# Optimization experiments

Hardware: AMD Instinct MI355X
Metric: run time of the kernel (lower is better)

Reference implementation:

```python
import jax, jax.numpy as jnp
import numpy as np

DIM = 1024
HEADS = 16
DIM_HEAD = 64
NUM_FREQS = 16
INNER = HEADS * DIM_HEAD


def rotate_half(x):
    # matches torch: cat((-x[..., 1::2], x[..., ::2]), dim=-1)
    x1 = x[..., ::2]
    x2 = x[..., 1::2]
    return jnp.concatenate((-x2, x1), axis=-1)


def rope_fourier_cache(seq_len, head_dim, num_freqs):
    freqs = 10000.0 ** (-jnp.arange(0, head_dim, 2, dtype=jnp.float32) / head_dim)  # [hd/2]
    pos = jnp.arange(seq_len, dtype=jnp.float32)[:, None]  # [n,1]
    angles = pos * freqs  # [n, hd/2]
    sin = jnp.sin(angles)
    cos = jnp.cos(angles)
    # interleave-duplicate each value per pair: [n, hd]
    sin = jnp.stack([sin, sin], axis=-1).reshape(seq_len, head_dim)
    cos = jnp.stack([cos, cos], axis=-1).reshape(seq_len, head_dim)
    ffreqs = jnp.arange(1, num_freqs + 1, dtype=jnp.float32)  # [F]
    p = jnp.arange(seq_len, dtype=jnp.float32)[:, None]  # [n,1]
    fourier = jnp.concatenate([jnp.sin(p * ffreqs), jnp.cos(p * ffreqs)], axis=-1)  # [n, 2F]
    return sin, cos, fourier


def setup_inputs() -> dict:
    key = jax.random.key(0)
    ks = jax.random.split(key, 6)
    b, n = 4, 2048
    x = jax.random.normal(ks[0], (b, n, DIM), dtype=jnp.float32)
    w_qkv = jax.random.normal(ks[1], (3 * INNER, DIM), dtype=jnp.float32) * (DIM ** -0.5)
    w_fproj = jax.random.normal(ks[2], (DIM_HEAD, 2 * NUM_FREQS), dtype=jnp.float32) * ((2 * NUM_FREQS) ** -0.5)
    b_fproj = jax.random.normal(ks[3], (DIM_HEAD,), dtype=jnp.float32) * 0.02
    w_out = jax.random.normal(ks[4], (DIM, INNER), dtype=jnp.float32) * (INNER ** -0.5)
    b_out = jax.random.normal(ks[5], (DIM,), dtype=jnp.float32) * 0.02
    return {"x": x, "w_qkv": w_qkv, "w_fproj": w_fproj, "b_fproj": b_fproj,
            "w_out": w_out, "b_out": b_out}


def reference(x, w_qkv, w_fproj, b_fproj, w_out, b_out):
    b, n, _ = x.shape
    scale = DIM_HEAD ** -0.5
    qkv = x @ w_qkv.T  # [b, n, 3*inner]
    q, k, v = jnp.split(qkv, 3, axis=-1)
    def to_heads(t):
        return t.reshape(b, n, HEADS, DIM_HEAD).transpose(0, 2, 1, 3)  # [b,h,n,d]
    q, k, v = to_heads(q), to_heads(k), to_heads(v)
    sin, cos, fourier = rope_fourier_cache(n, DIM_HEAD, NUM_FREQS)
    fenc = fourier @ w_fproj.T + b_fproj  # [n, d]
    fenc = fenc[None, None]  # [1,1,n,d]
    q = q * cos + rotate_half(q) * sin + fenc
    k = k * cos + rotate_half(k) * sin + fenc
    dots = jnp.einsum('bhid,bhjd->bhij', q, k) * scale
    attn = jax.nn.softmax(dots, axis=-1)
    out = jnp.einsum('bhij,bhjd->bhid', attn, v)
    out = out.transpose(0, 2, 1, 3).reshape(b, n, INNER)
    return out @ w_out.T + b_out
```

## Files before the change

kernel.cpp:

```cpp
#include <hip/hip_runtime.h>
#include <math.h>

#define NB 4
#define SEQ 2048
#define DIMM 1024
#define NH 16
#define DHD 64
#define NFQ 16

typedef __bf16 bf16x8 __attribute__((ext_vector_type(8)));
typedef float f32x4 __attribute__((ext_vector_type(4)));
typedef float f32x16 __attribute__((ext_vector_type(16)));
typedef unsigned int u32x4 __attribute__((ext_vector_type(4)));

#if __has_builtin(__builtin_amdgcn_exp2f)
#define EXP2F(x) __builtin_amdgcn_exp2f(x)
#else
#define EXP2F(x) exp2f(x)
#endif

__device__ inline unsigned short f2bf(float f) {
  unsigned int u = __builtin_bit_cast(unsigned int, f);
  u += 0x7fffu + ((u >> 16) & 1u);
  return (unsigned short)(u >> 16);
}

#define GLL16(gp, lp) __builtin_amdgcn_global_load_lds( \
    (__attribute__((address_space(1))) void*)(gp), \
    (__attribute__((address_space(3))) void*)(lp), 16, 0, 0)

__global__ __launch_bounds__(64) void rope_tab_kernel(const float* __restrict__ w_fproj,
                                                      const float* __restrict__ b_fproj,
                                                      float4* __restrict__ tab) {
  const int pos = blockIdx.x;
  const int d = threadIdx.x;
  __shared__ float four[2 * NFQ];
  if (d < NFQ) {
    double a = (double)pos * (double)(d + 1);
    four[d] = (float)sin(a);
    four[d + NFQ] = (float)cos(a);
  }
  __syncthreads();
  float fe = b_fproj[d];
  const float* wr = w_fproj + d * 2 * NFQ;
#pragma unroll
  for (int j = 0; j < 2 * NFQ; ++j) fe += four[j] * wr[j];
  const int i = d >> 1;
  const double freq = exp(((double)(-2 * i)) / 64.0 * log(10000.0));
  const float angle = (float)pos * (float)freq;
  const float c = (float)cos((double)angle);
  const float s = (float)sin((double)angle);
  tab[(pos << 6) + d] = make_float4(c, s, fe, 0.f);
}

__global__ __launch_bounds__(256) void f2bf_kernel(const float* __restrict__ src,
                                                   unsigned short* __restrict__ dst, int n4) {
  for (int i = blockIdx.x * 256 + threadIdx.x; i < n4; i += gridDim.x * 256) {
    const float4 v = ((const float4*)src)[i];
    ushort4 o;
    o.x = f2bf(v.x); o.y = f2bf(v.y); o.z = f2bf(v.z); o.w = f2bf(v.w);
    ((ushort4*)dst)[i] = o;
  }
}

template<int EPI>
__global__ __launch_bounds__(256) void gemm_bt(const unsigned short* __restrict__ A,
                                               const unsigned short* __restrict__ Bw,
                                               int K,
                                               float* __restrict__ outF,
                                               unsigned short* __restrict__ outQ,
                                               unsigned short* __restrict__ outK,
                                               unsigned short* __restrict__ outV,
                                               const float4* __restrict__ tab,
                                               const float* __restrict__ bias,
                                               float qscale) {
  __shared__ __align__(16) unsigned short As[3][128 * 32];
  __shared__ __align__(16) unsigned short Bs[3][128 * 32];
  const int t = threadIdx.x, l = t & 63, w = t >> 6;
  const int wr = w >> 1, wc = w & 1;
  const int orig = blockIdx.x + gridDim.x * blockIdx.y;
  const int xcd = orig & 7, idx = orig >> 3;
  const int sc = idx >> 5, r5 = idx & 31;
  const int bm = ((xcd << 3) + (r5 >> 2)) * 128;
  const int bn = ((sc << 2) + (r5 & 3)) * 128;
  const f32x4 z = {0.f, 0.f, 0.f, 0.f};
  f32x4 acc[4][4];
#pragma unroll
  for (int m = 0; m < 4; ++m)
#pragma unroll
    for (int n = 0; n < 4; ++n) acc[m][n] = z;

  auto stage = [&](int k0, int buf) {
#pragma unroll
    for (int j = 0; j < 2; ++j) {
      const int Bb = w * 2048 + j * 1024 + l * 16;
      const int row = Bb >> 6, bin = Bb & 63;
      const int sb = bin ^ ((row & 3) << 4);
      GLL16(A  + (size_t)(bm + row) * K + k0 + (sb >> 1), (char*)(&As[buf][0]) + w * 2048 + j * 1024);
      GLL16(Bw + (size_t)(bn + row) * K + k0 + (sb >> 1), (char*)(&Bs[buf][0]) + w * 2048 + j * 1024);
    }
  };

  const int NT = K >> 5;
  stage(0, 0);
  if (NT > 1) stage(32, 1);
  if (NT > 2) stage(64, 2);
  int cur = 0;
  for (int it = 0; it < NT; ++it) {
    const int rem = NT - 1 - it;
    if (rem >= 2)      asm volatile("s_waitcnt vmcnt(8)" ::: "memory");
    else if (rem == 1) asm volatile("s_waitcnt vmcnt(4)" ::: "memory");
    else               asm volatile("s_waitcnt vmcnt(0)" ::: "memory");
    __builtin_amdgcn_s_barrier();

    bf16x8 af[4], bfr[4];
#pragma unroll
    for (int m = 0; m < 4; ++m) {
      const int row = wr * 64 + m * 16 + (l & 15);
      const int bin = ((l >> 4) * 16) ^ ((row & 3) << 4);
      af[m] = *(const bf16x8*)((const char*)(&As[cur][0]) + row * 64 + bin);
    }
#pragma unroll
    for (int n = 0; n < 4; ++n) {
      const int row = wc * 64 + n * 16 + (l & 15);
      const int bin = ((l >> 4) * 16) ^ ((row & 3) << 4);
      bfr[n] = *(const bf16x8*)((const char*)(&Bs[cur][0]) + row * 64 + bin);
    }
#pragma unroll
    for (int m = 0; m < 4; ++m)
#pragma unroll
      for (int n = 0; n < 4; ++n)
        acc[m][n] = __builtin_amdgcn_mfma_f32_16x16x32_bf16(af[m], bfr[n], acc[m][n], 0, 0, 0);

    asm volatile("s_waitcnt lgkmcnt(0)" ::: "memory");
    __builtin_amdgcn_s_barrier();
    if (it + 3 < NT) stage((it + 3) * 32, cur);
    cur = (cur == 2) ? 0 : cur + 1;
  }

  const int c = l & 15;
  if (EPI == 0) {
    const int which = bn >> 10;
    const int h = ((bn & 1023) >> 6) + wc;
    if (which == 2) {
#pragma unroll
      for (int m = 0; m < 4; ++m)
#pragma unroll
        for (int n = 0; n < 4; ++n) {
          const int d = n * 16 + c;
#pragma unroll
          for (int r = 0; r < 4; ++r) {
            const int mrow = bm + wr * 64 + m * 16 + (l >> 4) * 4 + r;
            const int b = mrow >> 11, pos = mrow & (SEQ - 1);
            outV[((size_t)(b * NH + h) * DHD + d) * SEQ + pos] = f2bf(acc[m][n][r]);
          }
        }
    } else {
      unsigned short* dst = (which == 0) ? outQ : outK;
      const float sc2 = (which == 0) ? qscale : 1.f;
      const int laneE = (l & 48) | ((2 * c) & 15);
      const int laneO = (l & 48) | ((2 * c + 1) & 15);
      const bool hi = (c >= 8);
#pragma unroll
      for (int m = 0; m < 4; ++m)
#pragma unroll
        for (int r = 0; r < 4; ++r) {
          const int mrow = bm + wr * 64 + m * 16 + (l >> 4) * 4 + r;
          const int b = mrow >> 11, pos = mrow & (SEQ - 1);
          const float V0 = acc[m][0][r], V1 = acc[m][1][r];
          const float V2 = acc[m][2][r], V3 = acc[m][3][r];
          const float e0 = __shfl(V0, laneE), e1 = __shfl(V1, laneE);
          const float e2 = __shfl(V2, laneE), e3 = __shfl(V3, laneE);
          const float o0 = __shfl(V0, laneO), o1 = __shfl(V1, laneO);
          const float o2 = __shfl(V2, laneO), o3 = __shfl(V3, laneO);
          const float rot0 = -(hi ? o1 : o0);
          const float rot1 = -(hi ? o3 : o2);
          const float rot2 =  (hi ? e1 : e0);
          const float rot3 =  (hi ? e3 : e2);
          const float4 t0 = tab[(pos << 6) + c];
          const float4 t1 = tab[(pos << 6) + 16 + c];
          const float4 t2 = tab[(pos << 6) + 32 + c];
          const float4 t3 = tab[(pos << 6) + 48 + c];
          unsigned short* drow = dst + ((size_t)(b * NH + h) * SEQ + pos) * DHD + c;
          drow[0]  = f2bf((V0 * t0.x + rot0 * t0.y + t0.z) * sc2);
          drow[16] = f2bf((V1 * t1.x + rot1 * t1.y + t1.z) * sc2);
          drow[32] = f2bf((V2 * t2.x + rot2 * t2.y + t2.z) * sc2);
          drow[48] = f2bf((V3 * t3.x + rot3 * t3.y + t3.z) * sc2);
        }
    }
  } else {
#pragma unroll
    for (int m = 0; m < 4; ++m)
#pragma unroll
      for (int n = 0; n < 4; ++n) {
        const int ncol = bn + wc * 64 + n * 16 + c;
        const float bb = bias[ncol];
#pragma unroll
        for (int r = 0; r < 4; ++r) {
          const int mrow = bm + wr * 64 + m * 16 + (l >> 4) * 4 + r;
          outF[(size_t)mrow * DIMM + ncol] = acc[m][n][r] + bb;
        }
      }
  }
}

__global__ __launch_bounds__(256, 4) void attn_kernel(const unsigned short* __restrict__ qbf,
                                                      const unsigned short* __restrict__ kbf,
                                                      const unsigned short* __restrict__ vt,
                                                      unsigned short* __restrict__ ao) {
  __shared__ __align__(16) unsigned short Ks[2][64 * 64], Vts[2][64 * 64];
  const int t = threadIdx.x, l = t & 63, w = t >> 6;
  const int G = l >> 5, c32 = l & 31;
  int flat = blockIdx.x + (blockIdx.y << 4);
  flat = (flat & 7) * 128 + (flat >> 3);
  const int q0 = (flat & 15) * 128;
  const int bh = flat >> 4;
  const int b = bh >> 4, h = bh & 15;
  const size_t hbase = (size_t)bh * SEQ * DHD;
  const int woff = w * 32;

  bf16x8 ones;
#pragma unroll
  for (int j = 0; j < 8; ++j) ones[j] = (__bf16)1.0f;

  auto stageKV = [&](int kt, int buf) {
#pragma unroll
    for (int j = 0; j < 2; ++j) {
      const int base = (w * 2 + j) * 1024;
      const int row = (base + l * 16) >> 7;
      const int sb = ((l & 7) * 16) ^ ((row & 7) << 4);
      GLL16(kbf + hbase + (size_t)(kt + row) * DHD + (sb >> 1),
            (char*)(&Ks[buf][0]) + base);
      GLL16(vt  + hbase + (size_t)row * SEQ + kt + (sb >> 1),
            (char*)(&Vts[buf][0]) + base);
    }
  };

  bf16x8 qf[4];
#pragma unroll
  for (int j = 0; j < 4; ++j)
    qf[j] = *(const bf16x8*)(qbf + hbase +
        (size_t)(q0 + woff + c32) * DHD + 16 * j + 8 * G);

  stageKV(0, 0);
  stageKV(64, 1);

  f32x16 of[2], lsum;
#pragma unroll
  for (int r = 0; r < 16; ++r) { of[0][r] = 0.f; of[1][r] = 0.f; lsum[r] = 0.f; }

  for (int kt = 0; kt < SEQ; kt += 64) {
    const int cur = (kt >> 6) & 1;
    if (kt + 64 < SEQ) asm volatile("s_waitcnt vmcnt(4)" ::: "memory");
    else               asm volatile("s_waitcnt vmcnt(0)" ::: "memory");
    __builtin_amdgcn_s_barrier();

    const char* Kc = (const char*)(&Ks[cur][0]);
    const char* Vc = (const char*)(&Vts[cur][0]);

#pragma unroll
    for (int ksub = 0; ksub < 2; ++ksub) {
      f32x16 sf;
#pragma unroll
      for (int r = 0; r < 16; ++r) sf[r] = 0.f;
      const int krow = ksub * 32 + c32;
      const int kswz = (krow & 7) << 4;
      __builtin_amdgcn_s_setprio(1);
#pragma unroll
      for (int j = 0; j < 4; ++j) {
        const bf16x8 kf = *(const bf16x8*)(Kc + krow * 128 + ((32 * j + 16 * G) ^ kswz));
        sf = __builtin_amdgcn_mfma_f32_32x32x16_bf16(kf, qf[j], sf, 0, 0, 0);
      }
      __builtin_amdgcn_s_setprio(0);

      float p[16];
#pragma unroll
      for (int r = 0; r < 16; ++r) p[r] = EXP2F(sf[r]);
      unsigned W[8];
#pragma unroll
      for (int a = 0; a < 4; ++a)
#pragma unroll
        for (int hh = 0; hh < 2; ++hh)
          asm("v_cvt_pk_bf16_f32 %0, %1, %2"
              : "=v"(W[a * 2 + hh]) : "v"(p[4 * a + 2 * hh]), "v"(p[4 * a + 2 * hh + 1]));
      bf16x8 pa[2];
#pragma unroll
      for (int m = 0; m < 2; ++m) {
        const unsigned sendA = G ? W[4 * m + 0] : W[4 * m + 2];
        const unsigned sendB = G ? W[4 * m + 1] : W[4 * m + 3];
        const unsigned rA = (unsigned)__shfl_xor((int)sendA, 32);
        const unsigned rB = (unsigned)__shfl_xor((int)sendB, 32);
        const unsigned w0 = G ? rA : W[4 * m + 0];
        const unsigned w1 = G ? rB : W[4 * m + 1];
        const unsigned w2 = G ? W[4 * m + 2] : rA;
        const unsigned w3 = G ? W[4 * m + 3] : rB;
        const u32x4 tmp = {w0, w1, w2, w3};
        pa[m] = __builtin_bit_cast(bf16x8, tmp);
      }

      const int vrow0 = c32, vrow1 = 32 + c32;
      const int vswz0 = (vrow0 & 7) << 4, vswz1 = (vrow1 & 7) << 4;
      __builtin_amdgcn_s_setprio(1);
#pragma unroll
      for (int m = 0; m < 2; ++m) {
        lsum = __builtin_amdgcn_mfma_f32_32x32x16_bf16(pa[m], ones, lsum, 0, 0, 0);
        const int vb = 64 * ksub + 32 * m + 16 * G;
        const bf16x8 vf0 = *(const bf16x8*)(Vc + vrow0 * 128 + (vb ^ vswz0));
        const bf16x8 vf1 = *(const bf16x8*)(Vc + vrow1 * 128 + (vb ^ vswz1));
        of[0] = __builtin_amdgcn_mfma_f32_32x32x16_bf16(pa[m], vf0, of[0], 0, 0, 0);
        of[1] = __builtin_amdgcn_mfma_f32_32x32x16_bf16(pa[m], vf1, of[1], 0, 0, 0);
      }
      __builtin_amdgcn_s_setprio(0);
    }

    asm volatile("s_waitcnt lgkmcnt(0)" ::: "memory");
    __builtin_amdgcn_s_barrier();
    if (kt + 128 < SEQ) stageKV(kt + 128, cur);
  }

#pragma unroll
  for (int r = 0; r < 16; ++r) {
    const int qrow = (r & 3) + 8 * (r >> 2) + 4 * G;
    const float inv = 1.f / lsum[r];
    const int pos = q0 + woff + qrow;
#pragma unroll
    for (int dg = 0; dg < 2; ++dg) {
      const int col = h * DHD + dg * 32 + c32;
      ao[((size_t)(b * SEQ + pos)) * DIMM + col] = f2bf(of[dg][r] * inv);
    }
  }
}

extern "C" void kernel_launch(void* const* d_in, const int* in_sizes, int n_in,
                              void* d_out, int out_size, void* d_ws, size_t ws_size,
                              hipStream_t stream) {
  const float* x       = (const float*)d_in[0];
  const float* w_qkv   = (const float*)d_in[1];
  const float* w_fproj = (const float*)d_in[2];
  const float* b_fproj = (const float*)d_in[3];
  const float* w_out   = (const float*)d_in[4];
  const float* b_out   = (const float*)d_in[5];
  char* ws = (char*)d_ws;

  unsigned short* qbf    = (unsigned short*)(ws);
  unsigned short* kbf    = (unsigned short*)(ws + 16777216);
  unsigned short* vt     = (unsigned short*)(ws + 33554432);
  unsigned short* xbf    = (unsigned short*)(ws + 50331648);
  unsigned short* aobf   = (unsigned short*)(ws + 67108864);
  unsigned short* wqkvbf = (unsigned short*)(ws + 83886080);
  unsigned short* woutbf = (unsigned short*)(ws + 90177536);
  float4*         tab    = (float4*)(ws + 92274688);

  const float kLog2e = 1.4426950408889634f;

  hipLaunchKernelGGL(rope_tab_kernel, dim3(SEQ), dim3(DHD), 0, stream, w_fproj, b_fproj, tab);
  hipLaunchKernelGGL(f2bf_kernel, dim3(2048), dim3(256), 0, stream, x, xbf, (NB*SEQ*DIMM)/4);
  hipLaunchKernelGGL(f2bf_kernel, dim3(768), dim3(256), 0, stream, w_qkv, wqkvbf, (3*DIMM*DIMM)/4);
  hipLaunchKernelGGL(f2bf_kernel, dim3(256), dim3(256), 0, stream, w_out, woutbf, (DIMM*DIMM)/4);
  hipLaunchKernelGGL((gemm_bt<0>), dim3(24, 64), dim3(256), 0, stream,
                     xbf, wqkvbf, DIMM, (float*)nullptr, qbf, kbf, vt, tab,
                     (const float*)nullptr, 0.125f * kLog2e);
  hipLaunchKernelGGL(attn_kernel, dim3(SEQ/128, NB*NH), dim3(256), 0, stream, qbf, kbf, vt, aobf);
  hipLaunchKernelGGL((gemm_bt<1>), dim3(8, 64), dim3(256), 0, stream,
                     aobf, woutbf, DIMM, (float*)d_out, (unsigned short*)nullptr,
                     (unsigned short*)nullptr, (unsigned short*)nullptr, (const float4*)nullptr,
                     b_out, 1.0f);
}
```

Baseline: 201.9 us.

## Shrink attention blocks, read K straight from global, merge bf16 conversion launches

The attention kernel now uses 128-thread blocks covering 64 query rows each, doubling the grid. Only V^T is staged in LDS, and each wave loads its K fragments directly from global memory into registers. The three fp32-to-bf16 conversion launches are merged into one kernel that dispatches on flat index. This aims to cut LDS traffic and launch overhead and raise occupancy, but K is now read from global per wave with no LDS sharing, and V loads per block double relative to the query rows they serve.

After: 248.3 us. 1.23x slower.

```diff
diff --git a/kernel.cpp b/kernel.cpp
--- a/kernel.cpp
+++ b/kernel.cpp
@@ -53,13 +53,22 @@
   tab[(pos << 6) + d] = make_float4(c, s, fe, 0.f);
 }
 
-__global__ __launch_bounds__(256) void f2bf_kernel(const float* __restrict__ src,
-                                                   unsigned short* __restrict__ dst, int n4) {
-  for (int i = blockIdx.x * 256 + threadIdx.x; i < n4; i += gridDim.x * 256) {
-    const float4 v = ((const float4*)src)[i];
+__global__ __launch_bounds__(256) void f2bf3_kernel(const float* __restrict__ s0,
+                                                    unsigned short* __restrict__ d0, int n0,
+                                                    const float* __restrict__ s1,
+                                                    unsigned short* __restrict__ d1, int n1,
+                                                    const float* __restrict__ s2,
+                                                    unsigned short* __restrict__ d2, int n2) {
+  const int total = n0 + n1 + n2;
+  for (int i = blockIdx.x * 256 + threadIdx.x; i < total; i += gridDim.x * 256) {
+    const float* s; unsigned short* d; int j = i;
+    if (j < n0) { s = s0; d = d0; }
+    else if ((j -= n0) < n1) { s = s1; d = d1; }
+    else { j -= n1; s = s2; d = d2; }
+    const float4 v = ((const float4*)s)[j];
     ushort4 o;
     o.x = f2bf(v.x); o.y = f2bf(v.y); o.z = f2bf(v.z); o.w = f2bf(v.w);
-    ((ushort4*)dst)[i] = o;
+    ((ushort4*)d)[j] = o;
   }
 }
 
@@ -204,17 +213,17 @@
   }
 }
 
-__global__ __launch_bounds__(256, 4) void attn_kernel(const unsigned short* __restrict__ qbf,
+__global__ __launch_bounds__(128, 4) void attn_kernel(const unsigned short* __restrict__ qbf,
                                                       const unsigned short* __restrict__ kbf,
                                                       const unsigned short* __restrict__ vt,
                                                       unsigned short* __restrict__ ao) {
-  __shared__ __align__(16) unsigned short Ks[2][64 * 64], Vts[2][64 * 64];
+  __shared__ __align__(16) unsigned short Vts[2][64 * 64];
   const int t = threadIdx.x, l = t & 63, w = t >> 6;
   const int G = l >> 5, c32 = l & 31;
-  int flat = blockIdx.x + (blockIdx.y << 4);
-  flat = (flat & 7) * 128 + (flat >> 3);
-  const int q0 = (flat & 15) * 128;
-  const int bh = flat >> 4;
+  int flat = blockIdx.x + (blockIdx.y << 5);
+  flat = (flat & 7) * 256 + (flat >> 3);
+  const int q0 = (flat & 31) * 64;
+  const int bh = flat >> 5;
   const int b = bh >> 4, h = bh & 15;
   const size_t hbase = (size_t)bh * SEQ * DHD;
   const int woff = w * 32;
@@ -223,15 +232,13 @@
 #pragma unroll
   for (int j = 0; j < 8; ++j) ones[j] = (__bf16)1.0f;
 
-  auto stageKV = [&](int kt, int buf) {
-#pragma unroll
-    for (int j = 0; j < 2; ++j) {
-      const int base = (w * 2 + j) * 1024;
+  auto stageV = [&](int kt, int buf) {
+#pragma unroll
+    for (int j = 0; j < 4; ++j) {
+      const int base = (w * 4 + j) * 1024;
       const int row = (base + l * 16) >> 7;
       const int sb = ((l & 7) * 16) ^ ((row & 7) << 4);
-      GLL16(kbf + hbase + (size_t)(kt + row) * DHD + (sb >> 1),
-            (char*)(&Ks[buf][0]) + base);
-      GLL16(vt  + hbase + (size_t)row * SEQ + kt + (sb >> 1),
+      GLL16(vt + hbase + (size_t)row * SEQ + kt + (sb >> 1),
             (char*)(&Vts[buf][0]) + base);
     }
   };
@@ -242,8 +249,8 @@
     qf[j] = *(const bf16x8*)(qbf + hbase +
         (size_t)(q0 + woff + c32) * DHD + 16 * j + 8 * G);
 
-  stageKV(0, 0);
-  stageKV(64, 1);
+  stageV(0, 0);
+  stageV(64, 1);
 
   f32x16 of[2], lsum;
 #pragma unroll
@@ -255,22 +262,23 @@
     else               asm volatile("s_waitcnt vmcnt(0)" ::: "memory");
     __builtin_amdgcn_s_barrier();
 
-    const char* Kc = (const char*)(&Ks[cur][0]);
     const char* Vc = (const char*)(&Vts[cur][0]);
 
 #pragma unroll
     for (int ksub = 0; ksub < 2; ++ksub) {
+      const unsigned short* krow_p = kbf + hbase +
+          (size_t)(kt + ksub * 32 + c32) * DHD + 8 * G;
+      bf16x8 kf[4];
+#pragma unroll
+      for (int j = 0; j < 4; ++j) kf[j] = *(const bf16x8*)(krow_p + 16 * j);
+
       f32x16 sf;
 #pragma unroll
       for (int r = 0; r < 16; ++r) sf[r] = 0.f;
-      const int krow = ksub * 32 + c32;
-      const int kswz = (krow & 7) << 4;
       __builtin_amdgcn_s_setprio(1);
 #pragma unroll
-      for (int j = 0; j < 4; ++j) {
-        const bf16x8 kf = *(const bf16x8*)(Kc + krow * 128 + ((32 * j + 16 * G) ^ kswz));
-        sf = __builtin_amdgcn_mfma_f32_32x32x16_bf16(kf, qf[j], sf, 0, 0, 0);
-      }
+      for (int j = 0; j < 4; ++j)
+        sf = __builtin_amdgcn_mfma_f32_32x32x16_bf16(kf[j], qf[j], sf, 0, 0, 0);
       __builtin_amdgcn_s_setprio(0);
 
       float p[16];
@@ -315,7 +323,7 @@
 
     asm volatile("s_waitcnt lgkmcnt(0)" ::: "memory");
     __builtin_amdgcn_s_barrier();
-    if (kt + 128 < SEQ) stageKV(kt + 128, cur);
+    if (kt + 128 < SEQ) stageV(kt + 128, cur);
   }
 
 #pragma unroll
@@ -354,13 +362,14 @@
   const float kLog2e = 1.4426950408889634f;
 
   hipLaunchKernelGGL(rope_tab_kernel, dim3(SEQ), dim3(DHD), 0, stream, w_fproj, b_fproj, tab);
-  hipLaunchKernelGGL(f2bf_kernel, dim3(2048), dim3(256), 0, stream, x, xbf, (NB*SEQ*DIMM)/4);
-  hipLaunchKernelGGL(f2bf_kernel, dim3(768), dim3(256), 0, stream, w_qkv, wqkvbf, (3*DIMM*DIMM)/4);
-  hipLaunchKernelGGL(f2bf_kernel, dim3(256), dim3(256), 0, stream, w_out, woutbf, (DIMM*DIMM)/4);
+  hipLaunchKernelGGL(f2bf3_kernel, dim3(2048), dim3(256), 0, stream,
+                     x, xbf, (NB*SEQ*DIMM)/4,
+                     w_qkv, wqkvbf, (3*DIMM*DIMM)/4,
+                     w_out, woutbf, (DIMM*DIMM)/4);
   hipLaunchKernelGGL((gemm_bt<0>), dim3(24, 64), dim3(256), 0, stream,
                      xbf, wqkvbf, DIMM, (float*)nullptr, qbf, kbf, vt, tab,
                      (const float*)nullptr, 0.125f * kLog2e);
-  hipLaunchKernelGGL(attn_kernel, dim3(SEQ/128, NB*NH), dim3(256), 0, stream, qbf, kbf, vt, aobf);
+  hipLaunchKernelGGL(attn_kernel, dim3(SEQ/64, NB*NH), dim3(128), 0, stream, qbf, kbf, vt, aobf);
   hipLaunchKernelGGL((gemm_bt<1>), dim3(8, 64), dim3(256), 0, stream,
                      aobf, woutbf, DIMM, (float*)d_out, (unsigned short*)nullptr,
                      (unsigned short*)nullptr, (unsigned short*)nullptr, (const float4*)nullptr,
```
